# Optimization experiments

Measured on AMD Instinct MI355X. Metric: run time of the kernel, lower is better.

Reference implementation:

```python
import jax, jax.numpy as jnp
import numpy as np

B, H, W, C = 2, 128, 128, 128
K = 3            # window_size
NB = K * K       # neighbor_count = 9
RP = 8           # relative_position_dim
HID = 128        # edge hidden = max(256//2, 128)
EIN = 3 * C + RP # edge_input_dim = 392
CLIP = 3.0
GEPS = 1e-06     # gate_eps
LNE = 1e-05      # LayerNorm eps


def _ln(x, g, b):
    m = x.mean(-1, keepdims=True)
    v = ((x - m) ** 2).mean(-1, keepdims=True)
    return (x - m) * jax.lax.rsqrt(v + LNE) * g + b


def setup_inputs() -> dict:
    key = jax.random.key(0)
    ks = jax.random.split(key, 12)
    f32 = jnp.float32
    inp = {
        'tokens': jax.random.normal(ks[0], (B, H, W, C), dtype=f32),
        'ln1_g': jnp.ones((C,), f32), 'ln1_b': jnp.zeros((C,), f32),
        'ln2_g': jnp.ones((C,), f32), 'ln2_b': jnp.zeros((C,), f32),
        'rel_pos': 0.02 * jax.random.normal(ks[1], (NB, RP), dtype=f32),
        'dW1': 0.01 * jax.random.normal(ks[2], (EIN, HID), dtype=f32),
        'db1': jnp.zeros((HID,), f32),
        'dW2': 0.01 * jax.random.normal(ks[3], (HID, 1), dtype=f32),
        'db2': jnp.zeros((1,), f32),
        'rW1': 0.01 * jax.random.normal(ks[4], (EIN, HID), dtype=f32),
        'rb1': jnp.zeros((HID,), f32),
        'rW2': 0.01 * jax.random.normal(ks[5], (HID, 1), dtype=f32),
        'rb2': jnp.zeros((1,), f32),
        'vW': 0.01 * jax.random.normal(ks[6], (C, C), dtype=f32),
        'vb': jnp.zeros((C,), f32),
        'oW': 0.01 * jax.random.normal(ks[7], (C, C), dtype=f32),
        'ob': jnp.zeros((C,), f32),
        'eml_gamma': jnp.asarray(0.1, f32),
        'eml_lam': jnp.asarray(1.0, f32),
        'eml_bias': jnp.asarray(-0.3, f32),
    }
    return inp


def _edge_mlp(x, W1, b1, W2, b2):
    h = jax.nn.gelu(jnp.einsum('blnd,dh->blnh', x, W1) + b1, approximate=False)
    return jnp.einsum('blnh,ho->blno', h, W2) + b2


def _forward(tokens, ln1_g, ln1_b, ln2_g, ln2_b, rel_pos, dW1, db1, dW2, db2,
             rW1, rb1, rW2, rb2, vW, vb, oW, ob, eml_gamma, eml_lam, eml_bias,
             warmup_eta=1.0):
    Bh, Hh, Wh, Ch = tokens.shape
    L = Hh * Wh
    normalized = _ln(tokens, ln1_g, ln1_b)
    flat = normalized.reshape(Bh, L, Ch)
    # Unfold(kernel=3, padding=1): gather 9 shifted views, then replicate torch's
    # reshape of the (C, 9)-ordered channel axis into (9, C).
    pad = jnp.pad(normalized, ((0, 0), (1, 1), (1, 1), (0, 0)))
    shifts = [pad[:, i:i + Hh, j:j + Wh, :] for i in range(K) for j in range(K)]
    nbhd = jnp.stack(shifts, axis=-1)                       # [B,H,W,C,9]
    nbhd = nbhd.reshape(Bh, L, Ch * NB).reshape(Bh, L, NB, Ch)  # torch reshape semantics
    center = jnp.broadcast_to(flat[:, :, None, :], nbhd.shape)
    rel = jnp.broadcast_to(rel_pos[None, None], (Bh, L, NB, rel_pos.shape[-1]))
    edge_features = jnp.concatenate([center, nbhd, center - nbhd, rel], axis=-1)
    drive = _edge_mlp(edge_features, dW1, db1, dW2, db2)[..., 0]        # [B,L,9]
    resistance = _edge_mlp(edge_features, rW1, rb1, rW2, rb2)[..., 0]   # [B,L,9]
    # EML unit (Ohm's-law style gate): clamp(eta*gamma*drive/(lambda*softplus(R)+eps)+bias)
    energy = jnp.clip(
        warmup_eta * (eml_gamma * drive) / (eml_lam * jax.nn.softplus(resistance) + GEPS)
        + eml_bias, -CLIP, CLIP)
    gate = jax.nn.sigmoid(energy)                                        # [B,L,9]
    values = jnp.einsum('blnc,cd->blnd', nbhd, vW) + vb                  # [B,L,9,C]
    gate_mass = jnp.maximum(gate.sum(axis=2), GEPS)                      # [B,L]
    message = jnp.einsum('bln,blnc->blc', gate, values) / gate_mass[..., None]
    update = (jnp.einsum('blc,cd->bld', message, oW) + ob).reshape(Bh, Hh, Wh, Ch)
    output = _ln(tokens + update, ln2_g, ln2_b)  # dropout is identity at eval
    return output


def reference(tokens, ln1_g, ln1_b, ln2_g, ln2_b, rel_pos, dW1, db1, dW2, db2,
              rW1, rb1, rW2, rb2, vW, vb, oW, ob, eml_gamma, eml_lam, eml_bias):
    return _forward(tokens, ln1_g, ln1_b, ln2_g, ln2_b, rel_pos, dW1, db1, dW2, db2,
                    rW1, rb1, rW2, rb2, vW, vb, oW, ob, eml_gamma, eml_lam, eml_bias)
```

## Files before the change

### kernel.cpp

```cpp
#include <hip/hip_runtime.h>


#define USHORT unsigned short
#define AW 152

typedef __attribute__((ext_vector_type(8)))  __bf16 v8bf;
typedef __attribute__((ext_vector_type(8)))  USHORT v8u;
typedef __attribute__((ext_vector_type(16))) float  v16f;

__device__ __forceinline__ USHORT f2bf(float f) {
    unsigned v; __builtin_memcpy(&v, &f, 4);
    v += 0x7FFFu + ((v >> 16) & 1u);
    return (USHORT)(v >> 16);
}

__global__ __launch_bounds__(256) void k_setup(
    const float* __restrict__ tok, const float* __restrict__ ln1g,
    const float* __restrict__ ln1b,
    const float* __restrict__ dW1, const float* __restrict__ db1,
    const float* __restrict__ rW1, const float* __restrict__ rb1,
    const float* __restrict__ rel, const float* __restrict__ dW2,
    const float* __restrict__ rW2, const float* __restrict__ vW,
    const float* __restrict__ vb,  const float* __restrict__ oW,
    USHORT* __restrict__ norm,
    USHORT* __restrict__ WnTg, USHORT* __restrict__ WcTg, USHORT* __restrict__ VTg,
    float* __restrict__ preg, float* __restrict__ vboWg, float* __restrict__ w2g)
{
    const int blk = blockIdx.x, t = threadIdx.x;
    if (blk >= 354) {
        const int p = (blk - 354) * 4 + (t >> 6);
        const int lane = t & 63;
        const float2 x = ((const float2*)(tok + (size_t)p * 128))[lane];
        float s = x.x + x.y;
        for (int m = 1; m < 64; m <<= 1) s += __shfl_xor(s, m);
        const float mean = s * (1.f / 128.f);
        const float d0 = x.x - mean, d1 = x.y - mean;
        float q = d0 * d0 + d1 * d1;
        for (int m = 1; m < 64; m <<= 1) q += __shfl_xor(q, m);
        const float rstd = rsqrtf(q * (1.f / 128.f) + 1e-5f);
        const float2 gg = ((const float2*)ln1g)[lane], bb = ((const float2*)ln1b)[lane];
        ((unsigned*)norm)[(size_t)p * 64 + lane] =
            (unsigned)f2bf(d0 * rstd * gg.x + bb.x) |
            ((unsigned)f2bf(d1 * rstd * gg.y + bb.y) << 16);
        return;
    }
    if (blk < 72) {
        int idx = blk * 256 + t;
        int n = ((idx >> 4) * 7282) >> 16;
        int k = idx - n * 144;
        int r = k >> 4, tt = k & 15, c2 = r + 9 * tt;
        float acc = 0.f;
        if (c2 < 128)
            for (int j = 0; j < 128; ++j) acc += vW[c2 * 128 + j] * oW[j * 128 + n];
        VTg[idx] = f2bf(acc);
    } else if (blk < 216) {
        int idx = (blk - 72) * 256 + t;
        int n = ((idx >> 4) * 7282) >> 16;
        int k = idx - n * 144;
        int r = k >> 4, tt = k & 15, c2 = r + 9 * tt;
        int col = n & 127;
        const float* W = (n < 128) ? dW1 : rW1;
        float val = 0.f;
        if (c2 < 128) val = W[(128 + c2) * 128 + col] - W[(256 + c2) * 128 + col];
        WnTg[idx] = f2bf(val);
    } else if (blk < 344) {
        int idx = (blk - 216) * 256 + t;
        int n = idx >> 7, c = idx & 127, col = n & 127;
        const float* W = (n < 128) ? dW1 : rW1;
        WcTg[idx] = f2bf(W[c * 128 + col] + W[(256 + c) * 128 + col]);
    } else if (blk < 353) {
        int n2 = blk - 344; int h = t;
        float acc;
        if (h < 128) {
            acc = db1[h];
            for (int r = 0; r < 8; ++r) acc += rel[n2 * 8 + r] * dW1[(384 + r) * 128 + h];
        } else {
            int hh = h - 128;
            acc = rb1[hh];
            for (int r = 0; r < 8; ++r) acc += rel[n2 * 8 + r] * rW1[(384 + r) * 128 + hh];
        }
        preg[n2 * 256 + h] = acc;
    } else {
        if (t < 128) {
            float acc = 0.f;
            for (int j = 0; j < 128; ++j) acc += vb[j] * oW[j * 128 + t];
            vboWg[t] = acc;
            w2g[t] = dW2[t];
            w2g[128 + t] = rW2[t];
        }
    }
}

__device__ __forceinline__ void gather_tile(
    USHORT* __restrict__ Ash, const USHORT* __restrict__ nb,
    int n2, int y, int bI, int tid)
{
    const int x = tid >> 2, q = tid & 3;
    #pragma unroll
    for (int r = 0; r < 9; ++r) {
        int u = 2 * n2 + r;
        int n = (u >= 18) ? (u - 18) : ((u >= 9) ? (u - 9) : u);
        int v = n2 * 128 + r;
        int c0 = (v * 7282) >> 16;
        int dyq = (n * 22) >> 6;
        int dx = n - 3 * dyq - 1;
        int dy = dyq - 1;
        int sy = y + dy, sx = x + dx;
        bool ok = ((unsigned)sy < 128u) && ((unsigned)sx < 128u);
        int e0 = (c0 & ~1) + 4 * q;
        size_t gidx = ((size_t)((bI * 128 + (ok ? sy : 0)) * 128 + (ok ? sx : 0))) * 128 + e0;
        const unsigned* gp = (const unsigned*)nb + (gidx >> 1);
        unsigned dw0 = gp[0], dw1 = gp[1];
        unsigned nxt = (unsigned)__shfl_down((int)dw0, 1);
        unsigned o0, o1;
        if (c0 & 1) { o0 = (dw0 >> 16) | (dw1 << 16); o1 = (dw1 >> 16) | (nxt << 16); }
        else        { o0 = dw0;                       o1 = dw1; }
        if (!ok) { o0 = 0u; o1 = 0u; }
        *(uint2*)(Ash + x * AW + 16 * r + 4 * q) = make_uint2(o0, o1);
    }
}

__global__ __launch_bounds__(512, 2) void k_edge(
    const float* __restrict__ tok, const float* __restrict__ ln2g,
    const float* __restrict__ ln2b, const USHORT* __restrict__ nb,
    const USHORT* __restrict__ WnTg, const USHORT* __restrict__ WcTg,
    const USHORT* __restrict__ VTg, const float* __restrict__ preg,
    const float* __restrict__ vboWg, const float* __restrict__ w2g,
    const float* __restrict__ db2p, const float* __restrict__ rb2p,
    const float* __restrict__ gmp, const float* __restrict__ lmp,
    const float* __restrict__ bip, const float* __restrict__ obp,
    float* __restrict__ out)
{
    extern __shared__ char smem[];
    USHORT* Wsh  = (USHORT*)smem;
    USHORT* Ash  = (USHORT*)(smem + 77824);
    USHORT* VTl  = (USHORT*)(smem + 116736);
    float*  w2L  = (float*)(smem + 155648);
    float*  dsum = (float*)(smem + 156672);
    float*  rsum = (float*)(smem + 157184);
    float*  gateL= (float*)(smem + 157696);
    float*  sgL  = (float*)(smem + 158208);
    float*  updF = (float*)smem;

    const int tid = threadIdx.x;
    const int lane = tid & 63, wave = tid >> 6, hi = lane >> 5, l31 = lane & 31;
    const int mw = wave & 1, nw = wave >> 1;
    const int blk = blockIdx.x;
    const int bI = blk >> 7;
    const int y = ((blk & 7) << 4) | ((blk >> 3) & 15);
    const int p0 = (bI * 128 + y) * 128;

    for (int i = tid; i < 4096; i += 512) {
        int n = i >> 4, kv = i & 15;
        *(v8u*)(Wsh + n * AW + kv * 8) = *(const v8u*)(WcTg + n * 128 + kv * 8);
    }
    for (int i = tid; i < 2048; i += 512) {
        int x = i >> 4, kv = i & 15;
        *(v8u*)(Ash + x * AW + kv * 8) = *(const v8u*)(nb + (size_t)(p0 + x) * 128 + kv * 8);
    }
    for (int i = tid; i < 2304; i += 512) {
        int n = (i * 3641) >> 16;
        int kv = i - n * 18;
        *(v8u*)(VTl + n * AW + kv * 8) = *(const v8u*)(VTg + n * 144 + kv * 8);
    }
    if (tid < 256) w2L[tid] = w2g[tid];
    if (tid < 128) { dsum[tid] = 0.f; rsum[tid] = 0.f; sgL[tid] = 0.f; }
    __syncthreads();

    v16f cp[2][2];
    #pragma unroll
    for (int a = 0; a < 2; ++a)
        for (int b = 0; b < 2; ++b)
            for (int e = 0; e < 16; ++e) cp[a][b][e] = 0.f;
    #pragma unroll
    for (int ks = 0; ks < 8; ++ks) {
        v8bf af0 = *(const v8bf*)(Ash + (mw * 64 + l31) * AW + ks * 16 + hi * 8);
        v8bf af1 = *(const v8bf*)(Ash + (mw * 64 + 32 + l31) * AW + ks * 16 + hi * 8);
        v8bf bf0 = *(const v8bf*)(Wsh + (nw * 64 + l31) * AW + ks * 16 + hi * 8);
        v8bf bf1 = *(const v8bf*)(Wsh + (nw * 64 + 32 + l31) * AW + ks * 16 + hi * 8);
        cp[0][0] = __builtin_amdgcn_mfma_f32_32x32x16_bf16(af0, bf0, cp[0][0], 0, 0, 0);
        cp[0][1] = __builtin_amdgcn_mfma_f32_32x32x16_bf16(af0, bf1, cp[0][1], 0, 0, 0);
        cp[1][0] = __builtin_amdgcn_mfma_f32_32x32x16_bf16(af1, bf0, cp[1][0], 0, 0, 0);
        cp[1][1] = __builtin_amdgcn_mfma_f32_32x32x16_bf16(af1, bf1, cp[1][1], 0, 0, 0);
    }
    __syncthreads();

    for (int i = tid; i < 4608; i += 512) {
        int n = (i * 3641) >> 16;
        int kv = i - n * 18;
        *(v8u*)(Wsh + n * AW + kv * 8) = *(const v8u*)(WnTg + n * 144 + kv * 8);
    }
    gather_tile(Ash, nb, 0, y, bI, tid);

    const float gmv = gmp[0], lmv = lmp[0], biv = bip[0];
    const float db2v = db2p[0], rb2v = rb2p[0];
    const float wv0 = w2L[nw * 64 + l31];
    const float wv1 = w2L[nw * 64 + 32 + l31];

    v16f acc3[2];
    #pragma unroll
    for (int a = 0; a < 2; ++a)
        for (int e = 0; e < 16; ++e) acc3[a][e] = 0.f;

    for (int n2 = 0; n2 < 9; ++n2) {
        const float pv0 = preg[n2 * 256 + nw * 64 + l31];
        const float pv1 = preg[n2 * 256 + nw * 64 + 32 + l31];
        __syncthreads();
        v16f acc[2][2];
        #pragma unroll
        for (int a = 0; a < 2; ++a)
            for (int b = 0; b < 2; ++b) acc[a][b] = cp[a][b];
        #pragma unroll
        for (int ks = 0; ks < 9; ++ks) {
            v8bf af0 = *(const v8bf*)(Ash + (mw * 64 + l31) * AW + ks * 16 + hi * 8);
            v8bf af1 = *(const v8bf*)(Ash + (mw * 64 + 32 + l31) * AW + ks * 16 + hi * 8);
            v8bf bf0 = *(const v8bf*)(Wsh + (nw * 64 + l31) * AW + ks * 16 + hi * 8);
            v8bf bf1 = *(const v8bf*)(Wsh + (nw * 64 + 32 + l31) * AW + ks * 16 + hi * 8);
            acc[0][0] = __builtin_amdgcn_mfma_f32_32x32x16_bf16(af0, bf0, acc[0][0], 0, 0, 0);
            acc[0][1] = __builtin_amdgcn_mfma_f32_32x32x16_bf16(af0, bf1, acc[0][1], 0, 0, 0);
            acc[1][0] = __builtin_amdgcn_mfma_f32_32x32x16_bf16(af1, bf0, acc[1][0], 0, 0, 0);
            acc[1][1] = __builtin_amdgcn_mfma_f32_32x32x16_bf16(af1, bf1, acc[1][1], 0, 0, 0);
        }
        #pragma unroll
        for (int mt = 0; mt < 2; ++mt) {
            float part[16];
            #pragma unroll
            for (int rr = 0; rr < 16; ++rr) {
                float h0 = acc[mt][0][rr] + pv0;
                float h1 = acc[mt][1][rr] + pv1;
                float s0 = __builtin_amdgcn_rcpf(1.f + __expf(-1.702f * h0));
                float s1 = __builtin_amdgcn_rcpf(1.f + __expf(-1.702f * h1));
                part[rr] = h0 * s0 * wv0 + h1 * s1 * wv1;
            }
            #pragma unroll
            for (int m = 1; m < 32; m <<= 1) {
                #pragma unroll
                for (int rr = 0; rr < 16; ++rr) part[rr] += __shfl_xor(part[rr], m);
            }
            if (l31 == 0) {
                float* tgt = (nw < 2) ? dsum : rsum;
                #pragma unroll
                for (int rr = 0; rr < 16; ++rr) {
                    int row = mw * 64 + mt * 32 + (rr & 3) + 8 * (rr >> 2) + 4 * hi;
                    atomicAdd(&tgt[row], part[rr]);
                }
            }
        }
        v16f P[2];
        #pragma unroll
        for (int a = 0; a < 2; ++a)
            for (int e = 0; e < 16; ++e) P[a][e] = 0.f;
        #pragma unroll
        for (int ks = 0; ks < 9; ++ks) {
            v8bf af0 = *(const v8bf*)(Ash + (mw * 64 + l31) * AW + ks * 16 + hi * 8);
            v8bf af1 = *(const v8bf*)(Ash + (mw * 64 + 32 + l31) * AW + ks * 16 + hi * 8);
            v8bf vf  = *(const v8bf*)(VTl + (nw * 32 + l31) * AW + ks * 16 + hi * 8);
            P[0] = __builtin_amdgcn_mfma_f32_32x32x16_bf16(af0, vf, P[0], 0, 0, 0);
            P[1] = __builtin_amdgcn_mfma_f32_32x32x16_bf16(af1, vf, P[1], 0, 0, 0);
        }
        __syncthreads();
        if (n2 < 8) gather_tile(Ash, nb, n2 + 1, y, bI, tid);
        if (tid < 128) {
            float d = dsum[tid] + db2v, rr = rsum[tid] + rb2v;
            float sp = fmaxf(rr, 0.f) + log1pf(__expf(-fabsf(rr)));
            float e = gmv * d / (lmv * sp + 1e-6f) + biv;
            e = fminf(fmaxf(e, -3.f), 3.f);
            float gt = 1.f / (1.f + __expf(-e));
            gateL[tid] = gt; sgL[tid] += gt;
            dsum[tid] = 0.f; rsum[tid] = 0.f;
        }
        __syncthreads();
        #pragma unroll
        for (int mt = 0; mt < 2; ++mt) {
            const float4* gq = (const float4*)&gateL[mw * 64 + mt * 32 + 4 * hi];
            float4 ga = gq[0], gb = gq[2], gc = gq[4], gd = gq[6];
            float gs[16] = {ga.x, ga.y, ga.z, ga.w, gb.x, gb.y, gb.z, gb.w,
                            gc.x, gc.y, gc.z, gc.w, gd.x, gd.y, gd.z, gd.w};
            #pragma unroll
            for (int rr = 0; rr < 16; ++rr) acc3[mt][rr] += gs[rr] * P[mt][rr];
        }
    }

    if (tid < 128) {
        float s = sgL[tid];
        float m = fmaxf(s, 1e-6f);
        dsum[tid] = 1.f / m;
        rsum[tid] = s / m;
    }
    __syncthreads();

    {
        const int colc = nw * 32 + l31;
        const float vbw = vboWg[colc], obv = obp[colc];
        #pragma unroll
        for (int mt = 0; mt < 2; ++mt) {
            const int base = mw * 64 + mt * 32 + 4 * hi;
            const float4* iq = (const float4*)&dsum[base];
            const float4* sq = (const float4*)&rsum[base];
            float4 ia = iq[0], ib = iq[2], ic = iq[4], id = iq[6];
            float4 sa = sq[0], sb = sq[2], sc = sq[4], sd = sq[6];
            float iv[16] = {ia.x, ia.y, ia.z, ia.w, ib.x, ib.y, ib.z, ib.w,
                            ic.x, ic.y, ic.z, ic.w, id.x, id.y, id.z, id.w};
            float sv[16] = {sa.x, sa.y, sa.z, sa.w, sb.x, sb.y, sb.z, sb.w,
                            sc.x, sc.y, sc.z, sc.w, sd.x, sd.y, sd.z, sd.w};
            #pragma unroll
            for (int rr = 0; rr < 16; ++rr) {
                int row = base + (rr & 3) + 8 * (rr >> 2);
                updF[row * 128 + colc] = acc3[mt][rr] * iv[rr] + vbw * sv[rr] + obv;
            }
        }
    }
    __syncthreads();

    const float g20 = ln2g[lane], g21 = ln2g[lane + 64];
    const float b20 = ln2b[lane], b21 = ln2b[lane + 64];
    for (int q2 = 0; q2 < 16; ++q2) {
        int p = wave * 16 + q2;
        size_t gp = (size_t)(p0 + p) * 128;
        float x0 = tok[gp + lane]      + updF[p * 128 + lane];
        float x1 = tok[gp + lane + 64] + updF[p * 128 + lane + 64];
        float s = x0 + x1;
        for (int m = 1; m < 64; m <<= 1) s += __shfl_xor(s, m);
        float mean = s * (1.f / 128.f);
        float d0 = x0 - mean, d1 = x1 - mean;
        float qq = d0 * d0 + d1 * d1;
        for (int m = 1; m < 64; m <<= 1) qq += __shfl_xor(qq, m);
        float rstd = rsqrtf(qq * (1.f / 128.f) + 1e-5f);
        out[gp + lane]      = d0 * rstd * g20 + b20;
        out[gp + lane + 64] = d1 * rstd * g21 + b21;
    }
}

extern "C" void kernel_launch(void* const* d_in, const int* in_sizes, int n_in,
                              void* d_out, int out_size, void* d_ws, size_t ws_size,
                              hipStream_t stream) {
    const float* tok  = (const float*)d_in[0];
    const float* ln1g = (const float*)d_in[1];
    const float* ln1b = (const float*)d_in[2];
    const float* ln2g = (const float*)d_in[3];
    const float* ln2b = (const float*)d_in[4];
    const float* rel  = (const float*)d_in[5];
    const float* dW1  = (const float*)d_in[6];
    const float* db1  = (const float*)d_in[7];
    const float* dW2  = (const float*)d_in[8];
    const float* db2  = (const float*)d_in[9];
    const float* rW1  = (const float*)d_in[10];
    const float* rb1  = (const float*)d_in[11];
    const float* rW2  = (const float*)d_in[12];
    const float* rb2  = (const float*)d_in[13];
    const float* vW   = (const float*)d_in[14];
    const float* vb   = (const float*)d_in[15];
    const float* oW   = (const float*)d_in[16];
    const float* ob   = (const float*)d_in[17];
    const float* gm   = (const float*)d_in[18];
    const float* lm   = (const float*)d_in[19];
    const float* bi   = (const float*)d_in[20];
    float* out = (float*)d_out;

    char* w = (char*)d_ws;
    USHORT* norm = (USHORT*)w; w += 8388608;
    USHORT* WnTg = (USHORT*)w; w += 73728;
    USHORT* WcTg = (USHORT*)w; w += 65536;
    USHORT* VTg  = (USHORT*)w; w += 36864;
    float*  preg = (float*)w;  w += 9216;
    float*  vboWg= (float*)w;  w += 512;
    float*  w2g  = (float*)w;  w += 1024;

    hipFuncSetAttribute((const void*)k_edge,
                        hipFuncAttributeMaxDynamicSharedMemorySize, 158720);

    hipLaunchKernelGGL(k_setup, dim3(8546), dim3(256), 0, stream,
                       tok, ln1g, ln1b, dW1, db1, rW1, rb1, rel, dW2, rW2,
                       vW, vb, oW, norm, WnTg, WcTg, VTg, preg, vboWg, w2g);
    hipLaunchKernelGGL(k_edge, dim3(256), dim3(512), 158720, stream,
                       tok, ln2g, ln2b, norm, WnTg, WcTg, VTg, preg, vboWg, w2g,
                       db2, rb2, gm, lm, bi, ob, out);
}
```

Measured before the change: 208.3 us.

## Prefetch next neighbor gather into registers and use DPP reductions

Splits the neighbor gather into a global load into registers, issued at the top of each iteration, and a later LDS store after the MFMA work. The goal is to hide global-memory latency behind the edge MLP matmuls and to drop one barrier per iteration. It also replaces shfl_xor butterfly reductions with DPP row-shift/broadcast reductions for the per-row partial sums and the final LayerNorm. The prefetch costs 18 extra live registers per thread at 512 threads with 2 blocks per CU, so it may spill or pressure occupancy.

```diff
diff --git a/kernel.cpp b/kernel.cpp
--- a/kernel.cpp
+++ b/kernel.cpp
@@ -12,6 +12,28 @@
     unsigned v; __builtin_memcpy(&v, &f, 4);
     v += 0x7FFFu + ((v >> 16) & 1u);
     return (USHORT)(v >> 16);
+}
+
+template <int C>
+__device__ __forceinline__ float dpps(float x) {
+    return __int_as_float(
+        __builtin_amdgcn_update_dpp(0, __float_as_int(x), C, 0xf, 0xf, true));
+}
+__device__ __forceinline__ float red32half(float x) {
+    x += dpps<0x111>(x);
+    x += dpps<0x112>(x);
+    x += dpps<0x114>(x);
+    x += dpps<0x118>(x);
+    x += dpps<0x142>(x);
+    return x;
+}
+__device__ __forceinline__ float red64(float x) {
+    x = red32half(x);
+    x += dpps<0x143>(x);
+    return x;
+}
+__device__ __forceinline__ float bcast63(float x) {
+    return __int_as_float(__builtin_amdgcn_readlane(__float_as_int(x), 63));
 }
 
 __global__ __launch_bounds__(256) void k_setup(
@@ -91,8 +113,8 @@
     }
 }
 
-__device__ __forceinline__ void gather_tile(
-    USHORT* __restrict__ Ash, const USHORT* __restrict__ nb,
+__device__ __forceinline__ void gather_load(
+    uint2 (&pf)[9], const USHORT* __restrict__ nb,
     int n2, int y, int bI, int tid)
 {
     const int x = tid >> 2, q = tid & 3;
@@ -111,11 +133,24 @@
         size_t gidx = ((size_t)((bI * 128 + (ok ? sy : 0)) * 128 + (ok ? sx : 0))) * 128 + e0;
         const unsigned* gp = (const unsigned*)nb + (gidx >> 1);
         unsigned dw0 = gp[0], dw1 = gp[1];
+        pf[r].x = ok ? dw0 : 0u;
+        pf[r].y = ok ? dw1 : 0u;
+    }
+}
+
+__device__ __forceinline__ void gather_store(
+    USHORT* __restrict__ Ash, const uint2 (&pf)[9], int n2, int tid)
+{
+    const int x = tid >> 2, q = tid & 3;
+    #pragma unroll
+    for (int r = 0; r < 9; ++r) {
+        int v = n2 * 128 + r;
+        int c0 = (v * 7282) >> 16;
+        unsigned dw0 = pf[r].x, dw1 = pf[r].y;
         unsigned nxt = (unsigned)__shfl_down((int)dw0, 1);
         unsigned o0, o1;
         if (c0 & 1) { o0 = (dw0 >> 16) | (dw1 << 16); o1 = (dw1 >> 16) | (nxt << 16); }
         else        { o0 = dw0;                       o1 = dw1; }
-        if (!ok) { o0 = 0u; o1 = 0u; }
         *(uint2*)(Ash + x * AW + 16 * r + 4 * q) = make_uint2(o0, o1);
     }
 }
@@ -190,7 +225,11 @@
         int kv = i - n * 18;
         *(v8u*)(Wsh + n * AW + kv * 8) = *(const v8u*)(WnTg + n * 144 + kv * 8);
     }
-    gather_tile(Ash, nb, 0, y, bI, tid);
+    {
+        uint2 pf0[9];
+        gather_load(pf0, nb, 0, y, bI, tid);
+        gather_store(Ash, pf0, 0, tid);
+    }
 
     const float gmv = gmp[0], lmv = lmp[0], biv = bip[0];
     const float db2v = db2p[0], rb2v = rb2p[0];
@@ -202,10 +241,15 @@
     for (int a = 0; a < 2; ++a)
         for (int e = 0; e < 16; ++e) acc3[a][e] = 0.f;
 
+    __syncthreads();
+
     for (int n2 = 0; n2 < 9; ++n2) {
         const float pv0 = preg[n2 * 256 + nw * 64 + l31];
         const float pv1 = preg[n2 * 256 + nw * 64 + 32 + l31];
-        __syncthreads();
+
+        uint2 pf[9];
+        if (n2 < 8) gather_load(pf, nb, n2 + 1, y, bI, tid);
+
         v16f acc[2][2];
         #pragma unroll
         for (int a = 0; a < 2; ++a)
@@ -233,11 +277,8 @@
                 part[rr] = h0 * s0 * wv0 + h1 * s1 * wv1;
             }
             #pragma unroll
-            for (int m = 1; m < 32; m <<= 1) {
-                #pragma unroll
-                for (int rr = 0; rr < 16; ++rr) part[rr] += __shfl_xor(part[rr], m);
-            }
-            if (l31 == 0) {
+            for (int rr = 0; rr < 16; ++rr) part[rr] = red32half(part[rr]);
+            if (l31 == 31) {
                 float* tgt = (nw < 2) ? dsum : rsum;
                 #pragma unroll
                 for (int rr = 0; rr < 16; ++rr) {
@@ -259,7 +300,7 @@
             P[1] = __builtin_amdgcn_mfma_f32_32x32x16_bf16(af1, vf, P[1], 0, 0, 0);
         }
         __syncthreads();
-        if (n2 < 8) gather_tile(Ash, nb, n2 + 1, y, bI, tid);
+        if (n2 < 8) gather_store(Ash, pf, n2 + 1, tid);
         if (tid < 128) {
             float d = dsum[tid] + db2v, rr = rsum[tid] + rb2v;
             float sp = fmaxf(rr, 0.f) + log1pf(__expf(-fabsf(rr)));
@@ -319,13 +360,9 @@
         size_t gp = (size_t)(p0 + p) * 128;
         float x0 = tok[gp + lane]      + updF[p * 128 + lane];
         float x1 = tok[gp + lane + 64] + updF[p * 128 + lane + 64];
-        float s = x0 + x1;
-        for (int m = 1; m < 64; m <<= 1) s += __shfl_xor(s, m);
-        float mean = s * (1.f / 128.f);
+        float mean = bcast63(red64(x0 + x1)) * (1.f / 128.f);
         float d0 = x0 - mean, d1 = x1 - mean;
-        float qq = d0 * d0 + d1 * d1;
-        for (int m = 1; m < 64; m <<= 1) qq += __shfl_xor(qq, m);
-        float rstd = rsqrtf(qq * (1.f / 128.f) + 1e-5f);
+        float rstd = rsqrtf(bcast63(red64(d0 * d0 + d1 * d1)) * (1.f / 128.f) + 1e-5f);
         out[gp + lane]      = d0 * rstd * g20 + b20;
         out[gp + lane + 64] = d1 * rstd * g21 + b21;
     }
```

New measurement: 185.5 us. -11.0%, faster.
